# Optimization experiments

Measured on AMD Instinct MI355X. Metric: run time of the kernel, lower is better.

Reference implementation:

```python
import jax, jax.numpy as jnp
import numpy as np

N_NODES = 100000
N_EDGES = 1600000
IN_DIM = 128
HID_DIM = 128
OUT_DIM = 64


def _glorot(key, shape):
    fan_in, fan_out = shape
    lim = float(np.sqrt(6.0 / (fan_in + fan_out)))
    return jax.random.uniform(key, shape, jnp.float32, -lim, lim)


def setup_inputs() -> dict:
    key = jax.random.key(0)
    ks = jax.random.split(key, 8)
    x = jax.random.normal(ks[0], (N_NODES, IN_DIM), jnp.float32)
    edge_index = jax.random.randint(ks[1], (2, N_EDGES), 0, N_NODES, jnp.int64)
    edge_weight = jax.random.uniform(ks[2], (N_EDGES,), jnp.float32)
    W1 = _glorot(ks[3], (IN_DIM, HID_DIM))
    b1 = jnp.zeros((HID_DIM,), jnp.float32)
    W2 = _glorot(ks[4], (HID_DIM, HID_DIM))
    b2 = jnp.zeros((HID_DIM,), jnp.float32)
    W3 = _glorot(ks[5], (HID_DIM, OUT_DIM))
    b3 = jnp.zeros((OUT_DIM,), jnp.float32)
    return {"x": x, "edge_index": edge_index, "edge_weight": edge_weight,
            "W1": W1, "b1": b1, "W2": W2, "b2": b2, "W3": W3, "b3": b3}


def gcn_conv(x, src, dst, ew, W, b, n_nodes):
    # torch_geometric GCNConv: add self-loops (weight 1), symmetric normalization,
    # linear transform (no bias) then aggregate, then add bias.
    xw = x @ W                                            # [N, out]
    deg = jax.ops.segment_sum(ew, dst, num_segments=n_nodes) + 1.0  # self-loop
    dis = jax.lax.rsqrt(deg)                              # deg >= 1, safe
    norm = dis[src] * ew * dis[dst]                       # [E]
    agg = jax.ops.segment_sum(norm[:, None] * xw[src], dst, num_segments=n_nodes)
    # self-loop contribution: norm_ii = dis_i^2 * 1.0
    return agg + (dis * dis)[:, None] * xw + b


def reference(x, edge_index, edge_weight, W1, b1, W2, b2, W3, b3):
    src, dst = edge_index[0], edge_index[1]
    n = x.shape[0]
    h = gcn_conv(x, src, dst, edge_weight, W1, b1, n)
    h = jax.nn.relu(h)  # dropout is identity at inference
    h = gcn_conv(h, src, dst, edge_weight, W2, b2, n)
    h = jax.nn.relu(h)
    out = gcn_conv(h, src, dst, edge_weight, W3, b3, n)
    return out
```

## Files before the change

### kernel.cpp

```cpp
#include <hip/hip_runtime.h>


typedef __attribute__((ext_vector_type(8))) short bf16x8;
typedef __attribute__((ext_vector_type(4))) float f32x4;

__device__ inline unsigned short f2bf(float f) {
  unsigned int u = __float_as_uint(f);
  u += 0x7fffu + ((u >> 16) & 1u);
  return (unsigned short)(u >> 16);
}

__global__ void init_kernel(const int* __restrict__ ei, int* __restrict__ flag,
                            int* __restrict__ pz, int n) {
  if (blockIdx.x == 0) {
    __shared__ int nonzero;
    if (threadIdx.x == 0) nonzero = 0;
    __syncthreads();
    int acc = 0;
#pragma unroll
    for (int it = 0; it < 8; ++it) {
      const int j = threadIdx.x + (it << 8);
      acc |= ei[2 * j + 1];
    }
    if (acc != 0) atomicOr(&nonzero, 1);
    __syncthreads();
    if (threadIdx.x == 0) flag[0] = (nonzero == 0) ? 1 : 0;
  }
  int i = blockIdx.x * blockDim.x + threadIdx.x;
  const int stride = gridDim.x * blockDim.x;
  for (; i < n; i += stride) pz[i] = 0;
}

__global__ void count_deg_pack(const int* __restrict__ ei, const int* __restrict__ flag,
                               const float* __restrict__ ew,
                               unsigned long long* __restrict__ packed,
                               int* __restrict__ eseq, int E) {
  const int e = blockIdx.x * blockDim.x + threadIdx.x;
  if (e >= E) return;
  const int use64 = flag[0];
  const int d = use64 ? ei[2 * (E + e)] : ei[E + e];
  const unsigned int fx = (unsigned int)(ew[e] * 16777216.0f);
  const unsigned long long old =
      atomicAdd(&packed[d], (1ULL << 32) | (unsigned long long)fx);
  eseq[e] = (int)(old >> 32);
}

__global__ __launch_bounds__(256)
void scan_phase1(const unsigned long long* __restrict__ packed,
                 int* __restrict__ bsums, int N) {
  __shared__ int red[256];
  const int t = threadIdx.x;
  const int base = blockIdx.x * 1024 + t * 4;
  int s = 0;
#pragma unroll
  for (int j = 0; j < 4; ++j) {
    const int idx = base + j;
    if (idx < N) s += (int)(packed[idx] >> 32);
  }
  red[t] = s;
  __syncthreads();
  for (int off = 128; off > 0; off >>= 1) {
    if (t < off) red[t] += red[t + off];
    __syncthreads();
  }
  if (t == 0) bsums[blockIdx.x] = red[0];
}

__global__ __launch_bounds__(1024)
void scan_phase2(int* __restrict__ bsums, int* __restrict__ row_start, int B, int N) {
  __shared__ int s[1024];
  const int t = threadIdx.x;
  const int v = (t < B) ? bsums[t] : 0;
  s[t] = v;
  __syncthreads();
  for (int off = 1; off < 1024; off <<= 1) {
    const int add = (t >= off) ? s[t - off] : 0;
    __syncthreads();
    s[t] += add;
    __syncthreads();
  }
  if (t < B) bsums[t] = s[t] - v;
  if (t == B - 1) row_start[N] = s[t];
}

__global__ __launch_bounds__(256)
void scan_phase3_dis(const unsigned long long* __restrict__ packed,
                     const int* __restrict__ bsums, int* __restrict__ row_start,
                     float* __restrict__ dis, int N) {
  __shared__ int tsum[256];
  const int t = threadIdx.x;
  const int base = blockIdx.x * 1024 + t * 4;
  unsigned long long pk[4];
  int v[4];
#pragma unroll
  for (int j = 0; j < 4; ++j) {
    pk[j] = (base + j < N) ? packed[base + j] : 0ULL;
    v[j] = (int)(pk[j] >> 32);
  }
  const int tot = v[0] + v[1] + v[2] + v[3];
  tsum[t] = tot;
  __syncthreads();
  for (int off = 1; off < 256; off <<= 1) {
    const int add = (t >= off) ? tsum[t - off] : 0;
    __syncthreads();
    tsum[t] += add;
    __syncthreads();
  }
  int run = bsums[blockIdx.x] + tsum[t] - tot;
#pragma unroll
  for (int j = 0; j < 4; ++j) {
    const int idx = base + j;
    if (idx < N) {
      row_start[idx] = run;
      run += v[j];
      const float deg = (float)(unsigned int)pk[j] * (1.0f / 16777216.0f);
      dis[idx] = rsqrtf(deg + 1.0f);
    }
  }
}

__global__ void fill_csr(const int* __restrict__ ei, const int* __restrict__ flag,
                         const float* __restrict__ ew, const float* __restrict__ dis,
                         const int* __restrict__ row_start, const int* __restrict__ eseq,
                         int2* __restrict__ csr, int E) {
  const int e = blockIdx.x * blockDim.x + threadIdx.x;
  if (e >= E) return;
  const int use64 = flag[0];
  const int s = use64 ? ei[2 * e] : ei[e];
  const int d = use64 ? ei[2 * (E + e)] : ei[E + e];
  const float nm = dis[s] * ew[e] * dis[d];
  const int pos = row_start[d] + eseq[e];
  csr[pos] = make_int2(s, __float_as_int(nm));
}

__global__ __launch_bounds__(256)
void prep_bf16(const float* __restrict__ W1, const float* __restrict__ W2,
               const float* __restrict__ W3, unsigned short* __restrict__ Wt1,
               unsigned short* __restrict__ Wt2, unsigned short* __restrict__ Wt3,
               const float* __restrict__ x, unsigned short* __restrict__ xbf,
               long long n4) {
  const int WTB = 160;
  if (blockIdx.x < WTB) {
    const int idx = blockIdx.x * 256 + threadIdx.x;
    if (idx < 16384) {
      const int m = idx >> 7, k = idx & 127;
      Wt1[idx] = f2bf(W1[k * 128 + m]);
    } else if (idx < 32768) {
      const int l = idx - 16384;
      const int m = l >> 7, k = l & 127;
      Wt2[l] = f2bf(W2[k * 128 + m]);
    } else {
      const int l = idx - 32768;
      const int m = l >> 7, k = l & 127;
      Wt3[l] = f2bf(W3[k * 64 + m]);
    }
    return;
  }
  long long i = (long long)(blockIdx.x - WTB) * 256 + threadIdx.x;
  const long long stride = (long long)(gridDim.x - WTB) * 256;
  for (; i < n4; i += stride) {
    const float4 v = ((const float4*)x)[i];
    ushort4 o;
    o.x = f2bf(v.x); o.y = f2bf(v.y); o.z = f2bf(v.z); o.w = f2bf(v.w);
    ((ushort4*)xbf)[i] = o;
  }
}

template <int M>
__global__ __launch_bounds__(256)
void gemm_mfma(const unsigned short* __restrict__ A, const unsigned short* __restrict__ Bt,
               unsigned short* __restrict__ C, int N) {
  const int lane = threadIdx.x & 63;
  const int m = lane & 15;
  const int q = lane >> 4;
  const int row0 = (blockIdx.x << 6) + ((threadIdx.x >> 6) << 4);

  const bool rowok = (row0 + m) < N;
  const unsigned short* arow = A + (long long)(row0 + m) * 128 + q * 8;
  bf16x8 a[4];
  const bf16x8 zf = {0, 0, 0, 0, 0, 0, 0, 0};
#pragma unroll
  for (int kt = 0; kt < 4; ++kt)
    a[kt] = rowok ? *(const bf16x8*)(arow + kt * 32) : zf;

#pragma unroll
  for (int ct = 0; ct < M / 16; ++ct) {
    f32x4 acc = {0.f, 0.f, 0.f, 0.f};
    const unsigned short* brow = Bt + (ct * 16 + m) * 128 + q * 8;
#pragma unroll
    for (int kt = 0; kt < 4; ++kt) {
      const bf16x8 b = *(const bf16x8*)(brow + kt * 32);
      acc = __builtin_amdgcn_mfma_f32_16x16x32_bf16(a[kt], b, acc, 0, 0, 0);
    }
#pragma unroll
    for (int r = 0; r < 4; ++r) {
      const int row = row0 + q * 4 + r;
      if (row < N) C[(long long)row * M + ct * 16 + m] = f2bf(acc[r]);
    }
  }
}

template <int M, bool RELU, bool OUTBF>
__global__ __launch_bounds__(256)
void gather(const int2* __restrict__ csr, const int* __restrict__ row_start,
            const unsigned short* __restrict__ xw, const float* __restrict__ dis,
            const float* __restrict__ bias, void* __restrict__ outp, int N) {
  const int node = (blockIdx.x << 2) + (threadIdx.x >> 6);
  const int lane = threadIdx.x & 63;
  if (node >= N) return;
  const int beg = __builtin_amdgcn_readfirstlane(row_start[node]);
  const int end = __builtin_amdgcn_readfirstlane(row_start[node + 1]);
  if (M == 128) {
    const int c = lane << 1;
    float2 a0 = make_float2(0.f, 0.f), a1 = a0, a2 = a0, a3 = a0;
    int e = beg;
    for (; e + 7 < end; e += 8) {
      int2 p[8];
      unsigned int u[8];
#pragma unroll
      for (int j = 0; j < 8; ++j) p[j] = csr[e + j];
#pragma unroll
      for (int j = 0; j < 8; ++j)
        u[j] = *(const unsigned int*)(xw + (long long)p[j].x * 128 + c);
#pragma unroll
      for (int j = 0; j < 8; ++j) {
        const float nm = __int_as_float(p[j].y);
        float2& ac = (j & 4) ? ((j & 2) ? a3 : a2) : ((j & 2) ? a1 : a0);
        ac.x = fmaf(nm, __uint_as_float(u[j] << 16), ac.x);
        ac.y = fmaf(nm, __uint_as_float(u[j] & 0xffff0000u), ac.y);
      }
    }
    for (; e + 1 < end; e += 2) {
      const int2 p0 = csr[e], p1 = csr[e + 1];
      const unsigned int u0 = *(const unsigned int*)(xw + (long long)p0.x * 128 + c);
      const unsigned int u1 = *(const unsigned int*)(xw + (long long)p1.x * 128 + c);
      const float n0 = __int_as_float(p0.y), n1 = __int_as_float(p1.y);
      a0.x = fmaf(n0, __uint_as_float(u0 << 16), a0.x);
      a0.y = fmaf(n0, __uint_as_float(u0 & 0xffff0000u), a0.y);
      a1.x = fmaf(n1, __uint_as_float(u1 << 16), a1.x);
      a1.y = fmaf(n1, __uint_as_float(u1 & 0xffff0000u), a1.y);
    }
    if (e < end) {
      const int2 p = csr[e];
      const float nm = __int_as_float(p.y);
      const unsigned int u = *(const unsigned int*)(xw + (long long)p.x * 128 + c);
      a2.x = fmaf(nm, __uint_as_float(u << 16), a2.x);
      a2.y = fmaf(nm, __uint_as_float(u & 0xffff0000u), a2.y);
    }
    float2 acc;
    acc.x = (a0.x + a1.x) + (a2.x + a3.x);
    acc.y = (a0.y + a1.y) + (a2.y + a3.y);
    const float di = dis[node];
    const float dsq = di * di;
    const unsigned int su = *(const unsigned int*)(xw + (long long)node * 128 + c);
    const float2 bv = *(const float2*)(bias + c);
    acc.x = fmaf(dsq, __uint_as_float(su << 16), acc.x) + bv.x;
    acc.y = fmaf(dsq, __uint_as_float(su & 0xffff0000u), acc.y) + bv.y;
    if (RELU) { acc.x = fmaxf(acc.x, 0.f); acc.y = fmaxf(acc.y, 0.f); }
    if (OUTBF) {
      const unsigned int pk =
          (unsigned int)f2bf(acc.x) | ((unsigned int)f2bf(acc.y) << 16);
      ((unsigned int*)outp)[(long long)node * 64 + lane] = pk;
    } else {
      *(float2*)((float*)outp + (long long)node * 128 + c) = acc;
    }
  } else {
    float a0 = 0.f, a1 = 0.f, a2 = 0.f, a3 = 0.f;
    int e = beg;
    for (; e + 7 < end; e += 8) {
      int2 p[8];
      unsigned int v[8];
#pragma unroll
      for (int j = 0; j < 8; ++j) p[j] = csr[e + j];
#pragma unroll
      for (int j = 0; j < 8; ++j) v[j] = xw[(long long)p[j].x * 64 + lane];
#pragma unroll
      for (int j = 0; j < 8; ++j) {
        float& ac = (j & 4) ? ((j & 2) ? a3 : a2) : ((j & 2) ? a1 : a0);
        ac = fmaf(__int_as_float(p[j].y), __uint_as_float(v[j] << 16), ac);
      }
    }
    for (; e < end; ++e) {
      const int2 p = csr[e];
      const unsigned int v = xw[(long long)p.x * 64 + lane];
      a0 = fmaf(__int_as_float(p.y), __uint_as_float(v << 16), a0);
    }
    float acc = (a0 + a1) + (a2 + a3);
    const float di = dis[node];
    const unsigned int sv = xw[(long long)node * 64 + lane];
    float r = fmaf(di * di, __uint_as_float(sv << 16), acc) + bias[lane];
    if (RELU) r = fmaxf(r, 0.f);
    ((float*)outp)[(long long)node * 64 + lane] = r;
  }
}

extern "C" void kernel_launch(void* const* d_in, const int* in_sizes, int n_in,
                              void* d_out, int out_size, void* d_ws, size_t ws_size,
                              hipStream_t stream) {
  const float* x  = (const float*)d_in[0];
  const int*   ei = (const int*)d_in[1];
  const float* ew = (const float*)d_in[2];
  const float* W1 = (const float*)d_in[3];
  const float* b1 = (const float*)d_in[4];
  const float* W2 = (const float*)d_in[5];
  const float* b2 = (const float*)d_in[6];
  const float* W3 = (const float*)d_in[7];
  const float* b3 = (const float*)d_in[8];
  float* out = (float*)d_out;

  const int IN = 128;
  const int N = in_sizes[0] / IN;
  const int E = in_sizes[2];

  char* ws = (char*)d_ws;
  unsigned long long* packed = (unsigned long long*)(ws);
  float* dis       = (float*)(ws + (1u << 20));
  int*   flag      = (int*)(ws + (1536u << 10));
  int*   bsums     = (int*)(ws + (1536u << 10) + 4096);
  int*   row_start = (int*)(ws + (1600u << 10));
  int2*  csr       = (int2*)(ws + (2560u << 10));
  unsigned short* Wt1 = (unsigned short*)(ws + (15872u << 10));
  unsigned short* Wt2 = (unsigned short*)(ws + (15872u << 10) + (128u << 10));
  unsigned short* Wt3 = (unsigned short*)(ws + (15872u << 10) + (256u << 10));
  unsigned short* bufA = (unsigned short*)(ws + (16u << 20));
  unsigned short* hbf  = (unsigned short*)(ws + (42u << 20));
  int* eseq = (int*)bufA;

  const dim3 blk(256);
  const int gE = (E + 255) / 256;
  const int B = (N + 1023) / 1024;

  hipLaunchKernelGGL(init_kernel, dim3(128), blk, 0, stream, ei, flag, (int*)packed, 2 * N);
  hipLaunchKernelGGL(count_deg_pack, dim3(gE), blk, 0, stream, ei, flag, ew, packed, eseq, E);
  hipLaunchKernelGGL(scan_phase1, dim3(B), blk, 0, stream, packed, bsums, N);
  hipLaunchKernelGGL(scan_phase2, dim3(1), dim3(1024), 0, stream, bsums, row_start, B, N);
  hipLaunchKernelGGL(scan_phase3_dis, dim3(B), blk, 0, stream, packed, bsums, row_start, dis, N);
  hipLaunchKernelGGL(fill_csr, dim3(gE), blk, 0, stream, ei, flag, ew, dis, row_start, eseq, csr, E);
  hipLaunchKernelGGL(prep_bf16, dim3(160 + 2048), blk, 0, stream,
                     W1, W2, W3, Wt1, Wt2, Wt3, x, hbf, (long long)N * 32);

  const int gGemm = (N + 63) / 64;
  const int gGather = (N + 3) / 4;

  hipLaunchKernelGGL((gemm_mfma<128>), dim3(gGemm), blk, 0, stream, hbf, Wt1, bufA, N);
  hipLaunchKernelGGL((gather<128, true, true>), dim3(gGather), blk, 0, stream,
                     csr, row_start, bufA, dis, b1, hbf, N);
  hipLaunchKernelGGL((gemm_mfma<128>), dim3(gGemm), blk, 0, stream, hbf, Wt2, bufA, N);
  hipLaunchKernelGGL((gather<128, true, true>), dim3(gGather), blk, 0, stream,
                     csr, row_start, bufA, dis, b2, hbf, N);
  hipLaunchKernelGGL((gemm_mfma<64>), dim3(gGemm), blk, 0, stream, hbf, Wt3, bufA, N);
  hipLaunchKernelGGL((gather<64, false, false>), dim3(gGather), blk, 0, stream,
                     csr, row_start, bufA, dis, b3, out, N);
}
```

Measured before the change: 487.7 us.

## Merge independent preprocessing kernels into combined launches via block-range dispatch

Folds the degree-count kernel and the bf16 conversion of weights and x into one launch, and folds CSR fill with the first GEMM into another, using blockIdx ranges to select the role. This removes two kernel launches and lets independent work run concurrently on the GPU instead of serialising. eseq moves to its own workspace region so it no longer aliases bufA, which the first GEMM now writes in the same launch. The x-conversion part gets fewer blocks (1024 instead of 2048) and must loop more.

```diff
diff --git a/kernel.cpp b/kernel.cpp
--- a/kernel.cpp
+++ b/kernel.cpp
@@ -31,117 +31,28 @@
   for (; i < n; i += stride) pz[i] = 0;
 }
 
-__global__ void count_deg_pack(const int* __restrict__ ei, const int* __restrict__ flag,
-                               const float* __restrict__ ew,
-                               unsigned long long* __restrict__ packed,
-                               int* __restrict__ eseq, int E) {
-  const int e = blockIdx.x * blockDim.x + threadIdx.x;
-  if (e >= E) return;
-  const int use64 = flag[0];
-  const int d = use64 ? ei[2 * (E + e)] : ei[E + e];
-  const unsigned int fx = (unsigned int)(ew[e] * 16777216.0f);
-  const unsigned long long old =
-      atomicAdd(&packed[d], (1ULL << 32) | (unsigned long long)fx);
-  eseq[e] = (int)(old >> 32);
-}
-
-__global__ __launch_bounds__(256)
-void scan_phase1(const unsigned long long* __restrict__ packed,
-                 int* __restrict__ bsums, int N) {
-  __shared__ int red[256];
-  const int t = threadIdx.x;
-  const int base = blockIdx.x * 1024 + t * 4;
-  int s = 0;
-#pragma unroll
-  for (int j = 0; j < 4; ++j) {
-    const int idx = base + j;
-    if (idx < N) s += (int)(packed[idx] >> 32);
-  }
-  red[t] = s;
-  __syncthreads();
-  for (int off = 128; off > 0; off >>= 1) {
-    if (t < off) red[t] += red[t + off];
-    __syncthreads();
-  }
-  if (t == 0) bsums[blockIdx.x] = red[0];
-}
-
-__global__ __launch_bounds__(1024)
-void scan_phase2(int* __restrict__ bsums, int* __restrict__ row_start, int B, int N) {
-  __shared__ int s[1024];
-  const int t = threadIdx.x;
-  const int v = (t < B) ? bsums[t] : 0;
-  s[t] = v;
-  __syncthreads();
-  for (int off = 1; off < 1024; off <<= 1) {
-    const int add = (t >= off) ? s[t - off] : 0;
-    __syncthreads();
-    s[t] += add;
-    __syncthreads();
-  }
-  if (t < B) bsums[t] = s[t] - v;
-  if (t == B - 1) row_start[N] = s[t];
-}
-
-__global__ __launch_bounds__(256)
-void scan_phase3_dis(const unsigned long long* __restrict__ packed,
-                     const int* __restrict__ bsums, int* __restrict__ row_start,
-                     float* __restrict__ dis, int N) {
-  __shared__ int tsum[256];
-  const int t = threadIdx.x;
-  const int base = blockIdx.x * 1024 + t * 4;
-  unsigned long long pk[4];
-  int v[4];
-#pragma unroll
-  for (int j = 0; j < 4; ++j) {
-    pk[j] = (base + j < N) ? packed[base + j] : 0ULL;
-    v[j] = (int)(pk[j] >> 32);
-  }
-  const int tot = v[0] + v[1] + v[2] + v[3];
-  tsum[t] = tot;
-  __syncthreads();
-  for (int off = 1; off < 256; off <<= 1) {
-    const int add = (t >= off) ? tsum[t - off] : 0;
-    __syncthreads();
-    tsum[t] += add;
-    __syncthreads();
-  }
-  int run = bsums[blockIdx.x] + tsum[t] - tot;
-#pragma unroll
-  for (int j = 0; j < 4; ++j) {
-    const int idx = base + j;
-    if (idx < N) {
-      row_start[idx] = run;
-      run += v[j];
-      const float deg = (float)(unsigned int)pk[j] * (1.0f / 16777216.0f);
-      dis[idx] = rsqrtf(deg + 1.0f);
-    }
-  }
-}
-
-__global__ void fill_csr(const int* __restrict__ ei, const int* __restrict__ flag,
-                         const float* __restrict__ ew, const float* __restrict__ dis,
-                         const int* __restrict__ row_start, const int* __restrict__ eseq,
-                         int2* __restrict__ csr, int E) {
-  const int e = blockIdx.x * blockDim.x + threadIdx.x;
-  if (e >= E) return;
-  const int use64 = flag[0];
-  const int s = use64 ? ei[2 * e] : ei[e];
-  const int d = use64 ? ei[2 * (E + e)] : ei[E + e];
-  const float nm = dis[s] * ew[e] * dis[d];
-  const int pos = row_start[d] + eseq[e];
-  csr[pos] = make_int2(s, __float_as_int(nm));
-}
-
-__global__ __launch_bounds__(256)
-void prep_bf16(const float* __restrict__ W1, const float* __restrict__ W2,
-               const float* __restrict__ W3, unsigned short* __restrict__ Wt1,
-               unsigned short* __restrict__ Wt2, unsigned short* __restrict__ Wt3,
-               const float* __restrict__ x, unsigned short* __restrict__ xbf,
-               long long n4) {
-  const int WTB = 160;
-  if (blockIdx.x < WTB) {
-    const int idx = blockIdx.x * 256 + threadIdx.x;
+__global__ __launch_bounds__(256)
+void count_prep(const int* __restrict__ ei, const int* __restrict__ flag,
+                const float* __restrict__ ew, unsigned long long* __restrict__ packed,
+                int* __restrict__ eseq, int E, int gE,
+                const float* __restrict__ W1, const float* __restrict__ W2,
+                const float* __restrict__ W3, unsigned short* __restrict__ Wt1,
+                unsigned short* __restrict__ Wt2, unsigned short* __restrict__ Wt3,
+                const float* __restrict__ x, unsigned short* __restrict__ xbf,
+                long long n4) {
+  if (blockIdx.x < gE) {
+    const int e = blockIdx.x * 256 + threadIdx.x;
+    if (e >= E) return;
+    const int use64 = flag[0];
+    const int d = use64 ? ei[2 * (E + e)] : ei[E + e];
+    const unsigned int fx = (unsigned int)(ew[e] * 16777216.0f);
+    const unsigned long long old =
+        atomicAdd(&packed[d], (1ULL << 32) | (unsigned long long)fx);
+    eseq[e] = (int)(old >> 32);
+    return;
+  }
+  if (blockIdx.x < gE + 160) {
+    const int idx = (blockIdx.x - gE) * 256 + threadIdx.x;
     if (idx < 16384) {
       const int m = idx >> 7, k = idx & 127;
       Wt1[idx] = f2bf(W1[k * 128 + m]);
@@ -156,13 +67,135 @@
     }
     return;
   }
-  long long i = (long long)(blockIdx.x - WTB) * 256 + threadIdx.x;
-  const long long stride = (long long)(gridDim.x - WTB) * 256;
+  long long i = (long long)(blockIdx.x - gE - 160) * 256 + threadIdx.x;
+  const long long stride = (long long)(gridDim.x - gE - 160) * 256;
   for (; i < n4; i += stride) {
     const float4 v = ((const float4*)x)[i];
     ushort4 o;
     o.x = f2bf(v.x); o.y = f2bf(v.y); o.z = f2bf(v.z); o.w = f2bf(v.w);
     ((ushort4*)xbf)[i] = o;
+  }
+}
+
+__global__ __launch_bounds__(256)
+void scan_phase1(const unsigned long long* __restrict__ packed,
+                 int* __restrict__ bsums, int N) {
+  __shared__ int red[256];
+  const int t = threadIdx.x;
+  const int base = blockIdx.x * 1024 + t * 4;
+  int s = 0;
+#pragma unroll
+  for (int j = 0; j < 4; ++j) {
+    const int idx = base + j;
+    if (idx < N) s += (int)(packed[idx] >> 32);
+  }
+  red[t] = s;
+  __syncthreads();
+  for (int off = 128; off > 0; off >>= 1) {
+    if (t < off) red[t] += red[t + off];
+    __syncthreads();
+  }
+  if (t == 0) bsums[blockIdx.x] = red[0];
+}
+
+__global__ __launch_bounds__(1024)
+void scan_phase2(int* __restrict__ bsums, int* __restrict__ row_start, int B, int N) {
+  __shared__ int s[1024];
+  const int t = threadIdx.x;
+  const int v = (t < B) ? bsums[t] : 0;
+  s[t] = v;
+  __syncthreads();
+  for (int off = 1; off < 1024; off <<= 1) {
+    const int add = (t >= off) ? s[t - off] : 0;
+    __syncthreads();
+    s[t] += add;
+    __syncthreads();
+  }
+  if (t < B) bsums[t] = s[t] - v;
+  if (t == B - 1) row_start[N] = s[t];
+}
+
+__global__ __launch_bounds__(256)
+void scan_phase3_dis(const unsigned long long* __restrict__ packed,
+                     const int* __restrict__ bsums, int* __restrict__ row_start,
+                     float* __restrict__ dis, int N) {
+  __shared__ int tsum[256];
+  const int t = threadIdx.x;
+  const int base = blockIdx.x * 1024 + t * 4;
+  unsigned long long pk[4];
+  int v[4];
+#pragma unroll
+  for (int j = 0; j < 4; ++j) {
+    pk[j] = (base + j < N) ? packed[base + j] : 0ULL;
+    v[j] = (int)(pk[j] >> 32);
+  }
+  const int tot = v[0] + v[1] + v[2] + v[3];
+  tsum[t] = tot;
+  __syncthreads();
+  for (int off = 1; off < 256; off <<= 1) {
+    const int add = (t >= off) ? tsum[t - off] : 0;
+    __syncthreads();
+    tsum[t] += add;
+    __syncthreads();
+  }
+  int run = bsums[blockIdx.x] + tsum[t] - tot;
+#pragma unroll
+  for (int j = 0; j < 4; ++j) {
+    const int idx = base + j;
+    if (idx < N) {
+      row_start[idx] = run;
+      run += v[j];
+      const float deg = (float)(unsigned int)pk[j] * (1.0f / 16777216.0f);
+      dis[idx] = rsqrtf(deg + 1.0f);
+    }
+  }
+}
+
+__global__ __launch_bounds__(256)
+void fill_gemm1(const int* __restrict__ ei, const int* __restrict__ flag,
+                const float* __restrict__ ew, const float* __restrict__ dis,
+                const int* __restrict__ row_start, const int* __restrict__ eseq,
+                int2* __restrict__ csr, int E, int gE,
+                const unsigned short* __restrict__ A,
+                const unsigned short* __restrict__ Bt,
+                unsigned short* __restrict__ C, int N) {
+  if (blockIdx.x < gE) {
+    const int e = blockIdx.x * 256 + threadIdx.x;
+    if (e >= E) return;
+    const int use64 = flag[0];
+    const int s = use64 ? ei[2 * e] : ei[e];
+    const int d = use64 ? ei[2 * (E + e)] : ei[E + e];
+    const float nm = dis[s] * ew[e] * dis[d];
+    const int pos = row_start[d] + eseq[e];
+    csr[pos] = make_int2(s, __float_as_int(nm));
+    return;
+  }
+  const int bid = blockIdx.x - gE;
+  const int lane = threadIdx.x & 63;
+  const int m = lane & 15;
+  const int q = lane >> 4;
+  const int row0 = (bid << 6) + ((threadIdx.x >> 6) << 4);
+  const bool rowok = (row0 + m) < N;
+  const unsigned short* arow = A + (long long)(row0 + m) * 128 + q * 8;
+  bf16x8 a[4];
+  const bf16x8 zf = {0, 0, 0, 0, 0, 0, 0, 0};
+#pragma unroll
+  for (int kt = 0; kt < 4; ++kt)
+    a[kt] = rowok ? *(const bf16x8*)(arow + kt * 32) : zf;
+#pragma unroll
+  for (int ct = 0; ct < 8; ++ct) {
+    f32x4 acc = {0.f, 0.f, 0.f, 0.f};
+    const unsigned short* brow = Bt + (ct * 16 + m) * 128 + q * 8;
+#pragma unroll
+    for (int kt = 0; kt < 4; ++kt) {
+      const bf16x8 b = *(const bf16x8*)(brow + kt * 32);
+      acc = __builtin_amdgcn_mfma_f32_16x16x32_bf16(a[kt], b, acc, 0, 0, 0);
+    }
+#pragma unroll
+    for (int r = 0; r < 4; ++r) {
+      const int row = row0 + q * 4 + r;
+      if (row < N) C[(long long)row * 128 + ct * 16 + m] = f2bf(acc[r]);
+    }
   }
 }
 
@@ -324,25 +357,24 @@
   unsigned short* Wt3 = (unsigned short*)(ws + (15872u << 10) + (256u << 10));
   unsigned short* bufA = (unsigned short*)(ws + (16u << 20));
   unsigned short* hbf  = (unsigned short*)(ws + (42u << 20));
-  int* eseq = (int*)bufA;
+  int* eseq = (int*)(ws + (96u << 20));
 
   const dim3 blk(256);
   const int gE = (E + 255) / 256;
   const int B = (N + 1023) / 1024;
+  const int gGemm = (N + 63) / 64;
+  const int gGather = (N + 3) / 4;
 
   hipLaunchKernelGGL(init_kernel, dim3(128), blk, 0, stream, ei, flag, (int*)packed, 2 * N);
-  hipLaunchKernelGGL(count_deg_pack, dim3(gE), blk, 0, stream, ei, flag, ew, packed, eseq, E);
+  hipLaunchKernelGGL(count_prep, dim3(gE + 160 + 1024), blk, 0, stream,
+                     ei, flag, ew, packed, eseq, E, gE,
+                     W1, W2, W3, Wt1, Wt2, Wt3, x, hbf, (long long)N * 32);
   hipLaunchKernelGGL(scan_phase1, dim3(B), blk, 0, stream, packed, bsums, N);
   hipLaunchKernelGGL(scan_phase2, dim3(1), dim3(1024), 0, stream, bsums, row_start, B, N);
   hipLaunchKernelGGL(scan_phase3_dis, dim3(B), blk, 0, stream, packed, bsums, row_start, dis, N);
-  hipLaunchKernelGGL(fill_csr, dim3(gE), blk, 0, stream, ei, flag, ew, dis, row_start, eseq, csr, E);
-  hipLaunchKernelGGL(prep_bf16, dim3(160 + 2048), blk, 0, stream,
-                     W1, W2, W3, Wt1, Wt2, Wt3, x, hbf, (long long)N * 32);
-
-  const int gGemm = (N + 63) / 64;
-  const int gGather = (N + 3) / 4;
-
-  hipLaunchKernelGGL((gemm_mfma<128>), dim3(gGemm), blk, 0, stream, hbf, Wt1, bufA, N);
+  hipLaunchKernelGGL(fill_gemm1, dim3(gE + gGemm), blk, 0, stream,
+                     ei, flag, ew, dis, row_start, eseq, csr, E, gE,
+                     hbf, Wt1, bufA, N);
   hipLaunchKernelGGL((gather<128, true, true>), dim3(gGather), blk, 0, stream,
                      csr, row_start, bufA, dis, b1, hbf, N);
   hipLaunchKernelGGL((gemm_mfma<128>), dim3(gGemm), blk, 0, stream, hbf, Wt2, bufA, N);
```

Result: slower. 500.1 us (+2.5%).

## Split wavefront into two half-waves per edge pair in gather; merge init and prep kernels

Applied to the files above, without the earlier changes.

The gather kernel now has each half of a 64-lane wavefront handle alternate edges, with wider per-lane loads (8 bytes for the 128-wide layers, 4 bytes for the 64-wide layer). The two partial sums are combined with a cross-half shuffle, and only the lower half writes the result. This is meant to improve memory-level parallelism and load width in the bandwidth-bound sparse aggregation. Separately, the zero-init and bf16 conversion kernels are merged into one launch, and eseq is moved to its own workspace region so the conversion can run before the CSR build. The cost is some extra shuffle and reduction work, plus idle upper-half lanes during the store.

```diff
diff --git a/kernel.cpp b/kernel.cpp
--- a/kernel.cpp
+++ b/kernel.cpp
@@ -9,26 +9,58 @@
   u += 0x7fffu + ((u >> 16) & 1u);
   return (unsigned short)(u >> 16);
 }
-
-__global__ void init_kernel(const int* __restrict__ ei, int* __restrict__ flag,
-                            int* __restrict__ pz, int n) {
-  if (blockIdx.x == 0) {
+__device__ inline float bflo(unsigned int u) { return __uint_as_float(u << 16); }
+__device__ inline float bfhi(unsigned int u) { return __uint_as_float(u & 0xffff0000u); }
+
+__global__ __launch_bounds__(256)
+void init_prep(const int* __restrict__ ei, int* __restrict__ flag,
+               int* __restrict__ pz, int nz,
+               const float* __restrict__ W1, const float* __restrict__ W2,
+               const float* __restrict__ W3, unsigned short* __restrict__ Wt1,
+               unsigned short* __restrict__ Wt2, unsigned short* __restrict__ Wt3,
+               const float* __restrict__ x, unsigned short* __restrict__ xbf,
+               long long n4) {
+  const int r = blockIdx.x;
+  if (r == 0) {
     __shared__ int nonzero;
     if (threadIdx.x == 0) nonzero = 0;
     __syncthreads();
     int acc = 0;
 #pragma unroll
-    for (int it = 0; it < 8; ++it) {
-      const int j = threadIdx.x + (it << 8);
-      acc |= ei[2 * j + 1];
-    }
+    for (int it = 0; it < 8; ++it) acc |= ei[2 * (threadIdx.x + (it << 8)) + 1];
     if (acc != 0) atomicOr(&nonzero, 1);
     __syncthreads();
     if (threadIdx.x == 0) flag[0] = (nonzero == 0) ? 1 : 0;
   }
-  int i = blockIdx.x * blockDim.x + threadIdx.x;
-  const int stride = gridDim.x * blockDim.x;
-  for (; i < n; i += stride) pz[i] = 0;
+  if (r < 128) {
+    int i = r * 256 + threadIdx.x;
+    for (; i < nz; i += 128 * 256) pz[i] = 0;
+    return;
+  }
+  if (r < 288) {
+    const int idx = (r - 128) * 256 + threadIdx.x;
+    if (idx < 16384) {
+      const int m = idx >> 7, k = idx & 127;
+      Wt1[idx] = f2bf(W1[k * 128 + m]);
+    } else if (idx < 32768) {
+      const int l = idx - 16384;
+      const int m = l >> 7, k = l & 127;
+      Wt2[l] = f2bf(W2[k * 128 + m]);
+    } else if (idx < 40960) {
+      const int l = idx - 32768;
+      const int m = l >> 7, k = l & 127;
+      Wt3[l] = f2bf(W3[k * 64 + m]);
+    }
+    return;
+  }
+  long long i = (long long)(r - 288) * 256 + threadIdx.x;
+  const long long stride = (long long)(gridDim.x - 288) * 256;
+  for (; i < n4; i += stride) {
+    const float4 v = ((const float4*)x)[i];
+    ushort4 o;
+    o.x = f2bf(v.x); o.y = f2bf(v.y); o.z = f2bf(v.z); o.w = f2bf(v.w);
+    ((ushort4*)xbf)[i] = o;
+  }
 }
 
 __global__ void count_deg_pack(const int* __restrict__ ei, const int* __restrict__ flag,
@@ -133,39 +165,6 @@
   csr[pos] = make_int2(s, __float_as_int(nm));
 }
 
-__global__ __launch_bounds__(256)
-void prep_bf16(const float* __restrict__ W1, const float* __restrict__ W2,
-               const float* __restrict__ W3, unsigned short* __restrict__ Wt1,
-               unsigned short* __restrict__ Wt2, unsigned short* __restrict__ Wt3,
-               const float* __restrict__ x, unsigned short* __restrict__ xbf,
-               long long n4) {
-  const int WTB = 160;
-  if (blockIdx.x < WTB) {
-    const int idx = blockIdx.x * 256 + threadIdx.x;
-    if (idx < 16384) {
-      const int m = idx >> 7, k = idx & 127;
-      Wt1[idx] = f2bf(W1[k * 128 + m]);
-    } else if (idx < 32768) {
-      const int l = idx - 16384;
-      const int m = l >> 7, k = l & 127;
-      Wt2[l] = f2bf(W2[k * 128 + m]);
-    } else {
-      const int l = idx - 32768;
-      const int m = l >> 7, k = l & 127;
-      Wt3[l] = f2bf(W3[k * 64 + m]);
-    }
-    return;
-  }
-  long long i = (long long)(blockIdx.x - WTB) * 256 + threadIdx.x;
-  const long long stride = (long long)(gridDim.x - WTB) * 256;
-  for (; i < n4; i += stride) {
-    const float4 v = ((const float4*)x)[i];
-    ushort4 o;
-    o.x = f2bf(v.x); o.y = f2bf(v.y); o.z = f2bf(v.z); o.w = f2bf(v.w);
-    ((ushort4*)xbf)[i] = o;
-  }
-}
-
 template <int M>
 __global__ __launch_bounds__(256)
 void gemm_mfma(const unsigned short* __restrict__ A, const unsigned short* __restrict__ Bt,
@@ -202,95 +201,136 @@
 
 template <int M, bool RELU, bool OUTBF>
 __global__ __launch_bounds__(256)
-void gather(const int2* __restrict__ csr, const int* __restrict__ row_start,
-            const unsigned short* __restrict__ xw, const float* __restrict__ dis,
-            const float* __restrict__ bias, void* __restrict__ outp, int N) {
+void gather2(const int2* __restrict__ csr, const int* __restrict__ row_start,
+             const unsigned short* __restrict__ xw, const float* __restrict__ dis,
+             const float* __restrict__ bias, void* __restrict__ outp, int N) {
   const int node = (blockIdx.x << 2) + (threadIdx.x >> 6);
   const int lane = threadIdx.x & 63;
+  const int half = lane >> 5;
+  const int hl = lane & 31;
   if (node >= N) return;
   const int beg = __builtin_amdgcn_readfirstlane(row_start[node]);
   const int end = __builtin_amdgcn_readfirstlane(row_start[node + 1]);
   if (M == 128) {
-    const int c = lane << 1;
-    float2 a0 = make_float2(0.f, 0.f), a1 = a0, a2 = a0, a3 = a0;
+    const int c = hl << 2;
+    float4 A0 = make_float4(0.f, 0.f, 0.f, 0.f), A1 = A0, A2 = A0, A3 = A0;
     int e = beg;
     for (; e + 7 < end; e += 8) {
-      int2 p[8];
-      unsigned int u[8];
-#pragma unroll
-      for (int j = 0; j < 8; ++j) p[j] = csr[e + j];
-#pragma unroll
-      for (int j = 0; j < 8; ++j)
-        u[j] = *(const unsigned int*)(xw + (long long)p[j].x * 128 + c);
-#pragma unroll
-      for (int j = 0; j < 8; ++j) {
+      int2 p[4];
+      uint2 u[4];
+#pragma unroll
+      for (int j = 0; j < 4; ++j) p[j] = csr[e + 2 * j + half];
+#pragma unroll
+      for (int j = 0; j < 4; ++j)
+        u[j] = *(const uint2*)(xw + (long long)p[j].x * 128 + c);
+#pragma unroll
+      for (int j = 0; j < 4; ++j) {
         const float nm = __int_as_float(p[j].y);
-        float2& ac = (j & 4) ? ((j & 2) ? a3 : a2) : ((j & 2) ? a1 : a0);
-        ac.x = fmaf(nm, __uint_as_float(u[j] << 16), ac.x);
-        ac.y = fmaf(nm, __uint_as_float(u[j] & 0xffff0000u), ac.y);
+        float4& A = (j == 0) ? A0 : (j == 1) ? A1 : (j == 2) ? A2 : A3;
+        A.x = fmaf(nm, bflo(u[j].x), A.x);
+        A.y = fmaf(nm, bfhi(u[j].x), A.y);
+        A.z = fmaf(nm, bflo(u[j].y), A.z);
+        A.w = fmaf(nm, bfhi(u[j].y), A.w);
       }
     }
     for (; e + 1 < end; e += 2) {
-      const int2 p0 = csr[e], p1 = csr[e + 1];
-      const unsigned int u0 = *(const unsigned int*)(xw + (long long)p0.x * 128 + c);
-      const unsigned int u1 = *(const unsigned int*)(xw + (long long)p1.x * 128 + c);
-      const float n0 = __int_as_float(p0.y), n1 = __int_as_float(p1.y);
-      a0.x = fmaf(n0, __uint_as_float(u0 << 16), a0.x);
-      a0.y = fmaf(n0, __uint_as_float(u0 & 0xffff0000u), a0.y);
-      a1.x = fmaf(n1, __uint_as_float(u1 << 16), a1.x);
-      a1.y = fmaf(n1, __uint_as_float(u1 & 0xffff0000u), a1.y);
-    }
-    if (e < end) {
+      const int2 p = csr[e + half];
+      const uint2 u = *(const uint2*)(xw + (long long)p.x * 128 + c);
+      const float nm = __int_as_float(p.y);
+      A0.x = fmaf(nm, bflo(u.x), A0.x);
+      A0.y = fmaf(nm, bfhi(u.x), A0.y);
+      A0.z = fmaf(nm, bflo(u.y), A0.z);
+      A0.w = fmaf(nm, bfhi(u.y), A0.w);
+    }
+    if (e < end && half == 0) {
       const int2 p = csr[e];
+      const uint2 u = *(const uint2*)(xw + (long long)p.x * 128 + c);
       const float nm = __int_as_float(p.y);
-      const unsigned int u = *(const unsigned int*)(xw + (long long)p.x * 128 + c);
-      a2.x = fmaf(nm, __uint_as_float(u << 16), a2.x);
-      a2.y = fmaf(nm, __uint_as_float(u & 0xffff0000u), a2.y);
-    }
-    float2 acc;
-    acc.x = (a0.x + a1.x) + (a2.x + a3.x);
-    acc.y = (a0.y + a1.y) + (a2.y + a3.y);
+      A1.x = fmaf(nm, bflo(u.x), A1.x);
+      A1.y = fmaf(nm, bfhi(u.x), A1.y);
+      A1.z = fmaf(nm, bflo(u.y), A1.z);
+      A1.w = fmaf(nm, bfhi(u.y), A1.w);
+    }
+    float4 acc;
+    acc.x = (A0.x + A1.x) + (A2.x + A3.x);
+    acc.y = (A0.y + A1.y) + (A2.y + A3.y);
+    acc.z = (A0.z + A1.z) + (A2.z + A3.z);
+    acc.w = (A0.w + A1.w) + (A2.w + A3.w);
+    acc.x += __shfl_xor(acc.x, 32);
+    acc.y += __shfl_xor(acc.y, 32);
+    acc.z += __shfl_xor(acc.z, 32);
+    acc.w += __shfl_xor(acc.w, 32);
     const float di = dis[node];
     const float dsq = di * di;
-    const unsigned int su = *(const unsigned int*)(xw + (long long)node * 128 + c);
-    const float2 bv = *(const float2*)(bias + c);
-    acc.x = fmaf(dsq, __uint_as_float(su << 16), acc.x) + bv.x;
-    acc.y = fmaf(dsq, __uint_as_float(su & 0xffff0000u), acc.y) + bv.y;
-    if (RELU) { acc.x = fmaxf(acc.x, 0.f); acc.y = fmaxf(acc.y, 0.f); }
-    if (OUTBF) {
-      const unsigned int pk =
-          (unsigned int)f2bf(acc.x) | ((unsigned int)f2bf(acc.y) << 16);
-      ((unsigned int*)outp)[(long long)node * 64 + lane] = pk;
-    } else {
-      *(float2*)((float*)outp + (long long)node * 128 + c) = acc;
+    const uint2 su = *(const uint2*)(xw + (long long)node * 128 + c);
+    const float4 bv = *(const float4*)(bias + c);
+    acc.x = fmaf(dsq, bflo(su.x), acc.x) + bv.x;
+    acc.y = fmaf(dsq, bfhi(su.x), acc.y) + bv.y;
+    acc.z = fmaf(dsq, bflo(su.y), acc.z) + bv.z;
+    acc.w = fmaf(dsq, bfhi(su.y), acc.w) + bv.w;
+    if (RELU) {
+      acc.x = fmaxf(acc.x, 0.f); acc.y = fmaxf(acc.y, 0.f);
+      acc.z = fmaxf(acc.z, 0.f); acc.w = fmaxf(acc.w, 0.f);
+    }
+    if (half == 0) {
+      if (OUTBF) {
+        uint2 pk;
+        pk.x = (unsigned int)f2bf(acc.x) | ((unsigned int)f2bf(acc.y) << 16);
+        pk.y = (unsigned int)f2bf(acc.z) | ((unsigned int)f2bf(acc.w) << 16);
+        ((uint2*)outp)[(long long)node * 32 + hl] = pk;
+      } else {
+        *(float4*)((float*)outp + (long long)node * 128 + c) = acc;
+      }
     }
   } else {
-    float a0 = 0.f, a1 = 0.f, a2 = 0.f, a3 = 0.f;
+    const int c = hl << 1;
+    float2 A0 = make_float2(0.f, 0.f), A1 = A0, A2 = A0, A3 = A0;
     int e = beg;
     for (; e + 7 < end; e += 8) {
-      int2 p[8];
-      unsigned int v[8];
-#pragma unroll
-      for (int j = 0; j < 8; ++j) p[j] = csr[e + j];
-#pragma unroll
-      for (int j = 0; j < 8; ++j) v[j] = xw[(long long)p[j].x * 64 + lane];
-#pragma unroll
-      for (int j = 0; j < 8; ++j) {
-        float& ac = (j & 4) ? ((j & 2) ? a3 : a2) : ((j & 2) ? a1 : a0);
-        ac = fmaf(__int_as_float(p[j].y), __uint_as_float(v[j] << 16), ac);
+      int2 p[4];
+      unsigned int u[4];
+#pragma unroll
+      for (int j = 0; j < 4; ++j) p[j] = csr[e + 2 * j + half];
+#pragma unroll
+      for (int j = 0; j < 4; ++j)
+        u[j] = *(const unsigned int*)(xw + (long long)p[j].x * 64 + c);
+#pragma unroll
+      for (int j = 0; j < 4; ++j) {
+        const float nm = __int_as_float(p[j].y);
+        float2& A = (j == 0) ? A0 : (j == 1) ? A1 : (j == 2) ? A2 : A3;
+        A.x = fmaf(nm, bflo(u[j]), A.x);
+        A.y = fmaf(nm, bfhi(u[j]), A.y);
       }
     }
-    for (; e < end; ++e) {
+    for (; e + 1 < end; e += 2) {
+      const int2 p = csr[e + half];
+      const unsigned int u = *(const unsigned int*)(xw + (long long)p.x * 64 + c);
+      const float nm = __int_as_float(p.y);
+      A0.x = fmaf(nm, bflo(u), A0.x);
+      A0.y = fmaf(nm, bfhi(u), A0.y);
+    }
+    if (e < end && half == 0) {
       const int2 p = csr[e];
-      const unsigned int v = xw[(long long)p.x * 64 + lane];
-      a0 = fmaf(__int_as_float(p.y), __uint_as_float(v << 16), a0);
-    }
-    float acc = (a0 + a1) + (a2 + a3);
+      const unsigned int u = *(const unsigned int*)(xw + (long long)p.x * 64 + c);
+      const float nm = __int_as_float(p.y);
+      A1.x = fmaf(nm, bflo(u), A1.x);
+      A1.y = fmaf(nm, bfhi(u), A1.y);
+    }
+    float2 acc;
+    acc.x = (A0.x + A1.x) + (A2.x + A3.x);
+    acc.y = (A0.y + A1.y) + (A2.y + A3.y);
+    acc.x += __shfl_xor(acc.x, 32);
+    acc.y += __shfl_xor(acc.y, 32);
     const float di = dis[node];
-    const unsigned int sv = xw[(long long)node * 64 + lane];
-    float r = fmaf(di * di, __uint_as_float(sv << 16), acc) + bias[lane];
-    if (RELU) r = fmaxf(r, 0.f);
-    ((float*)outp)[(long long)node * 64 + lane] = r;
+    const float dsq = di * di;
+    const unsigned int sv = *(const unsigned int*)(xw + (long long)node * 64 + c);
+    const float2 bv = *(const float2*)(bias + c);
+    acc.x = fmaf(dsq, bflo(sv), acc.x) + bv.x;
+    acc.y = fmaf(dsq, bfhi(sv), acc.y) + bv.y;
+    if (RELU) { acc.x = fmaxf(acc.x, 0.f); acc.y = fmaxf(acc.y, 0.f); }
+    if (half == 0) {
+      *(float2*)((float*)outp + (long long)node * 64 + c) = acc;
+    }
   }
 }
 
@@ -324,31 +364,29 @@
   unsigned short* Wt3 = (unsigned short*)(ws + (15872u << 10) + (256u << 10));
   unsigned short* bufA = (unsigned short*)(ws + (16u << 20));
   unsigned short* hbf  = (unsigned short*)(ws + (42u << 20));
-  int* eseq = (int*)bufA;
+  int* eseq = (int*)(ws + (96u << 20));
 
   const dim3 blk(256);
   const int gE = (E + 255) / 256;
   const int B = (N + 1023) / 1024;
-
-  hipLaunchKernelGGL(init_kernel, dim3(128), blk, 0, stream, ei, flag, (int*)packed, 2 * N);
+  const int gGemm = (N + 63) / 64;
+  const int gGather = (N + 3) / 4;
+
+  hipLaunchKernelGGL(init_prep, dim3(288 + 1024), blk, 0, stream,
+                     ei, flag, (int*)packed, 2 * N,
+                     W1, W2, W3, Wt1, Wt2, Wt3, x, hbf, (long long)N * 32);
   hipLaunchKernelGGL(count_deg_pack, dim3(gE), blk, 0, stream, ei, flag, ew, packed, eseq, E);
   hipLaunchKernelGGL(scan_phase1, dim3(B), blk, 0, stream, packed, bsums, N);
   hipLaunchKernelGGL(scan_phase2, dim3(1), dim3(1024), 0, stream, bsums, row_start, B, N);
   hipLaunchKernelGGL(scan_phase3_dis, dim3(B), blk, 0, stream, packed, bsums, row_start, dis, N);
   hipLaunchKernelGGL(fill_csr, dim3(gE), blk, 0, stream, ei, flag, ew, dis, row_start, eseq, csr, E);
-  hipLaunchKernelGGL(prep_bf16, dim3(160 + 2048), blk, 0, stream,
-                     W1, W2, W3, Wt1, Wt2, Wt3, x, hbf, (long long)N * 32);
-
-  const int gGemm = (N + 63) / 64;
-  const int gGather = (N + 3) / 4;
-
   hipLaunchKernelGGL((gemm_mfma<128>), dim3(gGemm), blk, 0, stream, hbf, Wt1, bufA, N);
-  hipLaunchKernelGGL((gather<128, true, true>), dim3(gGather), blk, 0, stream,
+  hipLaunchKernelGGL((gather2<128, true, true>), dim3(gGather), blk, 0, stream,
                      csr, row_start, bufA, dis, b1, hbf, N);
   hipLaunchKernelGGL((gemm_mfma<128>), dim3(gGemm), blk, 0, stream, hbf, Wt2, bufA, N);
-  hipLaunchKernelGGL((gather<128, true, true>), dim3(gGather), blk, 0, stream,
+  hipLaunchKernelGGL((gather2<128, true, true>), dim3(gGather), blk, 0, stream,
                      csr, row_start, bufA, dis, b2, hbf, N);
   hipLaunchKernelGGL((gemm_mfma<64>), dim3(gGemm), blk, 0, stream, hbf, Wt3, bufA, N);
-  hipLaunchKernelGGL((gather<64, false, false>), dim3(gGather), blk, 0, stream,
+  hipLaunchKernelGGL((gather2<64, false, false>), dim3(gGather), blk, 0, stream,
                      csr, row_start, bufA, dis, b3, out, N);
 }
```

New measurement: 517.6 us. +6.1%, slower.
